# Performance work log

Measured on AMD Instinct MI355X. Metric: run time of the kernel, lower is better.

## Reference

```python
import jax, jax.numpy as jnp
import numpy as np

B, T, E = 4096, 200, 64
VOCAB_ITEM, VOCAB_USER, VOCAB_CTX = 100000, 100000, 10000
DENSE = 16
ATT_H1, ATT_H2 = 64, 32
MLP_H1, MLP_H2 = 256, 128
MLP_IN = E * 4 + DENSE  # 2 sparse feats + item_emb + interest_vec + dense


def _lin(key, fan_in, fan_out):
    k1, k2 = jax.random.split(key)
    s = 1.0 / np.sqrt(fan_in)
    w = jax.random.uniform(k1, (fan_in, fan_out), jnp.float32, -s, s)
    b = jax.random.uniform(k2, (fan_out,), jnp.float32, -s, s)
    return w, b


def setup_inputs() -> dict:
    key = jax.random.key(0)
    ks = jax.random.split(key, 16)
    inp = {}
    inp["target_item"] = jax.random.randint(ks[0], (B,), 0, VOCAB_ITEM)
    inp["history_items"] = jax.random.randint(ks[1], (B, T), 0, VOCAB_ITEM)
    inp["history_mask"] = jax.random.randint(ks[2], (B, T), 0, 2).astype(bool)
    sf_user = jax.random.randint(ks[3], (B, 1), 0, VOCAB_USER)
    sf_ctx = jax.random.randint(ks[4], (B, 1), 0, VOCAB_CTX)
    inp["sparse_features"] = jnp.concatenate([sf_user, sf_ctx], axis=1)
    inp["dense_features"] = jax.random.normal(ks[5], (B, DENSE), jnp.float32)
    # parameters
    inp["item_table"] = jax.random.normal(ks[6], (VOCAB_ITEM, E), jnp.float32)
    inp["user_table"] = jax.random.normal(ks[7], (VOCAB_USER, E), jnp.float32)
    inp["ctx_table"] = jax.random.normal(ks[8], (VOCAB_CTX, E), jnp.float32)
    inp["att_w1"], inp["att_b1"] = _lin(ks[9], 4 * E, ATT_H1)
    inp["att_w2"], inp["att_b2"] = _lin(ks[10], ATT_H1, ATT_H2)
    inp["att_wo"], inp["att_bo"] = _lin(ks[11], ATT_H2, 1)
    inp["mlp_w1"], inp["mlp_b1"] = _lin(ks[12], MLP_IN, MLP_H1)
    inp["mlp_w2"], inp["mlp_b2"] = _lin(ks[13], MLP_H1, MLP_H2)
    inp["out_w"], inp["out_b"] = _lin(ks[14], MLP_H2, 1)
    return inp


def reference(target_item, history_items, history_mask, sparse_features, dense_features,
              item_table, user_table, ctx_table,
              att_w1, att_b1, att_w2, att_b2, att_wo, att_bo,
              mlp_w1, mlp_b1, mlp_w2, mlp_b2, out_w, out_b):
    # embedding lookups
    q = item_table[target_item]               # (B, E)
    keys = item_table[history_items]          # (B, T, E)
    qe = jnp.broadcast_to(q[:, None, :], keys.shape)
    # local activation unit: concat(keys, query, diff, prod) -> small MLP -> score
    attn_in = jnp.concatenate([keys, qe, keys - qe, keys * qe], axis=-1)  # (B, T, 4E)
    h = jax.nn.relu(attn_in @ att_w1 + att_b1)
    h = jax.nn.relu(h @ att_w2 + att_b2)
    scores = (h @ att_wo + att_bo)[..., 0]    # (B, T)
    scores = jnp.where(history_mask, scores, -1e9)
    weights = jax.nn.softmax(scores, axis=-1)
    interest = jnp.einsum('bt,bte->be', weights, keys)  # (B, E)
    # other sparse features
    sp = jnp.concatenate([user_table[sparse_features[:, 0]],
                          ctx_table[sparse_features[:, 1]]], axis=-1)  # (B, 2E)
    mlp_in = jnp.concatenate([sp, q, interest, dense_features], axis=-1)  # (B, 4E+DENSE)
    h = jax.nn.relu(mlp_in @ mlp_w1 + mlp_b1)
    h = jax.nn.relu(h @ mlp_w2 + mlp_b2)
    logits = h @ out_w + out_b                # (B, 1)
    return logits
```

## Files before the change

kernel.cpp:

```cpp
#include <hip/hip_runtime.h>
#include <stdint.h>

#define NB 4096
#define NT 200
#define NE 64

typedef __attribute__((ext_vector_type(8))) __bf16 bf16x8;
typedef __attribute__((ext_vector_type(4))) __bf16 bf16x4;
typedef __attribute__((ext_vector_type(4))) float f32x4;

__device__ __forceinline__ void cvt8(const float4 a, const float4 b,
                                     bf16x8& hi, bf16x8& lo)
{
    float x[8] = {a.x, a.y, a.z, a.w, b.x, b.y, b.z, b.w};
#pragma unroll
    for (int i = 0; i < 8; ++i) {
        const __bf16 h = (__bf16)x[i];
        hi[i] = h;
        lo[i] = (__bf16)(x[i] - (float)h);
    }
}

struct __align__(16) SmemM {
    __bf16 wT_hi[64 * 72];
    __bf16 wT_lo[64 * 72];
    __bf16 w2T_hi[32 * 72];
    __bf16 w2T_lo[32 * 72];
    float  q[64];
    float  biasj[64];
    float  b2[32];
    float  wo[32];
    float  ip[8 * 64];
    float  red_a[8];
    float  red_b[8];
    float  scores[256];
    float  bounce[8][16 * 36];
};

__global__ __launch_bounds__(512)
void din_attn(const int* __restrict__ target_item,
              const int* __restrict__ history_items,
              const int* __restrict__ history_mask,
              const int* __restrict__ sparse_features,
              const float* __restrict__ dense_features,
              const float* __restrict__ item_table,
              const float* __restrict__ user_table,
              const float* __restrict__ ctx_table,
              const float* __restrict__ att_w1,
              const float* __restrict__ att_b1,
              const float* __restrict__ att_w2,
              const float* __restrict__ att_b2,
              const float* __restrict__ att_wo,
              const float* __restrict__ att_bo,
              float* __restrict__ mlp_in)
{
    __shared__ SmemM sm;

    const int b    = blockIdx.x;
    const int tid  = threadIdx.x;
    const int wv   = tid >> 6;
    const int lane = tid & 63;
    const int l15  = lane & 15;
    const int g4   = lane >> 4;

    bf16x8 khi[2][2], klo[2][2];
#pragma unroll
    for (int mt = 0; mt < 2; ++mt) {
        int t = 32 * wv + mt * 16 + l15;
        if (t > NT - 1) t = NT - 1;
        const int hr = history_items[(size_t)b * NT + t];
        const float* kp = item_table + (size_t)hr * NE + g4 * 8;
#pragma unroll
        for (int ks = 0; ks < 2; ++ks) {
            const float4 f0 = *(const float4*)(kp + ks * 32);
            const float4 f1 = *(const float4*)(kp + ks * 32 + 4);
            cvt8(f0, f1, khi[mt][ks], klo[mt][ks]);
        }
    }

    float pre_u = 0.f, pre_c = 0.f, pre_d = 0.f;
    if (tid < NE) {
        pre_u = user_table[(size_t)sparse_features[b * 2 + 0] * NE + tid];
        pre_c = ctx_table[(size_t)sparse_features[b * 2 + 1] * NE + tid];
    } else if (tid < 80) {
        pre_d = dense_features[(size_t)b * 16 + (tid - 64)];
    }

    if (tid < NE) sm.q[tid] = item_table[(size_t)target_item[b] * NE + tid];
    if (tid < 32) { sm.b2[tid] = att_b2[tid]; sm.wo[tid] = att_wo[tid]; }
    const float bo = att_bo[0];
    __syncthreads();

    {
        const int j  = tid & 63;
        const int eb = (tid >> 6) * 8;
        float pb = 0.f;
        bf16x8 vhi, vlo;
#pragma unroll
        for (int i = 0; i < 8; ++i) {
            const int e = eb + i;
            const float qe = sm.q[e];
            const float A  = att_w1[(size_t)(e)       * NE + j];
            const float Bv = att_w1[(size_t)(64 + e)  * NE + j];
            const float C  = att_w1[(size_t)(128 + e) * NE + j];
            const float D  = att_w1[(size_t)(192 + e) * NE + j];
            const float wf = A + C + qe * D;
            const __bf16 h = (__bf16)wf;
            vhi[i] = h;
            vlo[i] = (__bf16)(wf - (float)h);
            pb += qe * (Bv - C);
        }
        *(bf16x8*)(sm.wT_hi + (size_t)j * 72 + eb) = vhi;
        *(bf16x8*)(sm.wT_lo + (size_t)j * 72 + eb) = vlo;
        sm.ip[(tid >> 6) * 64 + j] = pb;
    }
    {
        const int o  = tid & 31;
        const int jb = (tid >> 5) * 4;
        bf16x4 vhi, vlo;
#pragma unroll
        for (int i = 0; i < 4; ++i) {
            const float v = att_w2[(size_t)(jb + i) * 32 + o];
            const __bf16 h = (__bf16)v;
            vhi[i] = h;
            vlo[i] = (__bf16)(v - (float)h);
        }
        *(bf16x4*)(sm.w2T_hi + (size_t)o * 72 + jb) = vhi;
        *(bf16x4*)(sm.w2T_lo + (size_t)o * 72 + jb) = vlo;
    }
    __syncthreads();
    if (tid < NE) {
        float s = att_b1[tid];
#pragma unroll
        for (int w = 0; w < 8; ++w) s += sm.ip[w * 64 + tid];
        sm.biasj[tid] = s;
    }
    __syncthreads();

    f32x4 acc1[2][4];
    {
        const f32x4 z = {0.f, 0.f, 0.f, 0.f};
#pragma unroll
        for (int mt = 0; mt < 2; ++mt)
#pragma unroll
            for (int nt = 0; nt < 4; ++nt) acc1[mt][nt] = z;
    }
#pragma unroll
    for (int nt = 0; nt < 4; ++nt) {
        const __bf16* bph = sm.wT_hi + (nt * 16 + l15) * 72 + g4 * 8;
        const __bf16* bpl = sm.wT_lo + (nt * 16 + l15) * 72 + g4 * 8;
        const bf16x8 bh0 = *(const bf16x8*)(bph);
        const bf16x8 bh1 = *(const bf16x8*)(bph + 32);
        const bf16x8 bl0 = *(const bf16x8*)(bpl);
        const bf16x8 bl1 = *(const bf16x8*)(bpl + 32);
#pragma unroll
        for (int mt = 0; mt < 2; ++mt) {
            f32x4 a = acc1[mt][nt];
            a = __builtin_amdgcn_mfma_f32_16x16x32_bf16(khi[mt][0], bh0, a, 0, 0, 0);
            a = __builtin_amdgcn_mfma_f32_16x16x32_bf16(khi[mt][0], bl0, a, 0, 0, 0);
            a = __builtin_amdgcn_mfma_f32_16x16x32_bf16(klo[mt][0], bh0, a, 0, 0, 0);
            a = __builtin_amdgcn_mfma_f32_16x16x32_bf16(khi[mt][1], bh1, a, 0, 0, 0);
            a = __builtin_amdgcn_mfma_f32_16x16x32_bf16(khi[mt][1], bl1, a, 0, 0, 0);
            a = __builtin_amdgcn_mfma_f32_16x16x32_bf16(klo[mt][1], bh1, a, 0, 0, 0);
            acc1[mt][nt] = a;
        }
    }

#pragma unroll
    for (int nt = 0; nt < 4; ++nt) {
        const float bj = sm.biasj[nt * 16 + l15];
#pragma unroll
        for (int mt = 0; mt < 2; ++mt)
#pragma unroll
            for (int r = 0; r < 4; ++r)
                acc1[mt][nt][r] = fmaxf(acc1[mt][nt][r] + bj, 0.f);
    }

    bf16x8 a2hi[2][2], a2lo[2][2];
    {
        float* bnc = sm.bounce[wv];
#pragma unroll
        for (int mt = 0; mt < 2; ++mt) {
#pragma unroll
            for (int k2s = 0; k2s < 2; ++k2s) {
#pragma unroll
                for (int ntl = 0; ntl < 2; ++ntl) {
                    const int nt = k2s * 2 + ntl;
#pragma unroll
                    for (int r = 0; r < 4; ++r)
                        bnc[(g4 * 4 + r) * 36 + ntl * 16 + l15] = acc1[mt][nt][r];
                }
                const float* rp = bnc + l15 * 36 + g4 * 8;
                const float4 u0 = *(const float4*)(rp);
                const float4 u1 = *(const float4*)(rp + 4);
                cvt8(u0, u1, a2hi[mt][k2s], a2lo[mt][k2s]);
            }
        }
    }

    f32x4 acc2[2][2];
    {
        const f32x4 z = {0.f, 0.f, 0.f, 0.f};
#pragma unroll
        for (int mt = 0; mt < 2; ++mt) { acc2[mt][0] = z; acc2[mt][1] = z; }
    }
#pragma unroll
    for (int nt2 = 0; nt2 < 2; ++nt2) {
        const __bf16* bph = sm.w2T_hi + (nt2 * 16 + l15) * 72 + g4 * 8;
        const __bf16* bpl = sm.w2T_lo + (nt2 * 16 + l15) * 72 + g4 * 8;
        const bf16x8 bh0 = *(const bf16x8*)(bph);
        const bf16x8 bh1 = *(const bf16x8*)(bph + 32);
        const bf16x8 bl0 = *(const bf16x8*)(bpl);
        const bf16x8 bl1 = *(const bf16x8*)(bpl + 32);
#pragma unroll
        for (int mt = 0; mt < 2; ++mt) {
            f32x4 a = acc2[mt][nt2];
            a = __builtin_amdgcn_mfma_f32_16x16x32_bf16(a2hi[mt][0], bh0, a, 0, 0, 0);
            a = __builtin_amdgcn_mfma_f32_16x16x32_bf16(a2hi[mt][0], bl0, a, 0, 0, 0);
            a = __builtin_amdgcn_mfma_f32_16x16x32_bf16(a2lo[mt][0], bh0, a, 0, 0, 0);
            a = __builtin_amdgcn_mfma_f32_16x16x32_bf16(a2hi[mt][1], bh1, a, 0, 0, 0);
            a = __builtin_amdgcn_mfma_f32_16x16x32_bf16(a2hi[mt][1], bl1, a, 0, 0, 0);
            a = __builtin_amdgcn_mfma_f32_16x16x32_bf16(a2lo[mt][1], bh1, a, 0, 0, 0);
            acc2[mt][nt2] = a;
        }
    }

    float sc[2][4];
#pragma unroll
    for (int mt = 0; mt < 2; ++mt)
#pragma unroll
        for (int r = 0; r < 4; ++r) sc[mt][r] = 0.f;
#pragma unroll
    for (int nt2 = 0; nt2 < 2; ++nt2) {
        const float bb = sm.b2[nt2 * 16 + l15];
        const float ww = sm.wo[nt2 * 16 + l15];
#pragma unroll
        for (int mt = 0; mt < 2; ++mt)
#pragma unroll
            for (int r = 0; r < 4; ++r)
                sc[mt][r] += fmaxf(acc2[mt][nt2][r] + bb, 0.f) * ww;
    }
#pragma unroll
    for (int mt = 0; mt < 2; ++mt)
#pragma unroll
        for (int r = 0; r < 4; ++r) {
            float v = sc[mt][r];
            v += __shfl_xor(v, 1);
            v += __shfl_xor(v, 2);
            v += __shfl_xor(v, 4);
            v += __shfl_xor(v, 8);
            sc[mt][r] = v;
        }
    if (l15 == 0) {
#pragma unroll
        for (int mt = 0; mt < 2; ++mt)
#pragma unroll
            for (int r = 0; r < 4; ++r) {
                const int t = 32 * wv + mt * 16 + g4 * 4 + r;
                float val;
                if (t < NT) {
                    const int mk = history_mask[(size_t)b * NT + t];
                    val = (mk != 0) ? (sc[mt][r] + bo) : -1e9f;
                } else {
                    val = -INFINITY;
                }
                sm.scores[t] = val;
            }
    }
    __syncthreads();

    const float v = (tid < 256) ? sm.scores[tid] : -INFINITY;
    float m = v;
#pragma unroll
    for (int s = 32; s; s >>= 1) m = fmaxf(m, __shfl_xor(m, s));
    if (lane == 0) sm.red_a[wv] = m;
    __syncthreads();
    float mx = sm.red_a[0];
#pragma unroll
    for (int w = 1; w < 8; ++w) mx = fmaxf(mx, sm.red_a[w]);
    const float ex = __expf(v - mx);
    float ssum = ex;
#pragma unroll
    for (int s = 32; s; s >>= 1) ssum += __shfl_xor(ssum, s);
    if (lane == 0) sm.red_b[wv] = ssum;
    __syncthreads();
    float total = 0.f;
#pragma unroll
    for (int w = 0; w < 8; ++w) total += sm.red_b[w];
    if (tid < 256) sm.scores[tid] = ex / total;
    __syncthreads();

    {
        const int e = lane;
        float acc = 0.f;
        const int tb = 25 * wv;
#pragma unroll 5
        for (int i = 0; i < 25; ++i) {
            const int t = tb + i;
            const float wt = sm.scores[t];
            const int hr = history_items[(size_t)b * NT + t];
            acc += wt * item_table[(size_t)hr * NE + e];
        }
        sm.ip[wv * 64 + e] = acc;
    }
    __syncthreads();

    float* row = mlp_in + (size_t)b * 272;
    if (tid < NE) {
        float inter = 0.f;
#pragma unroll
        for (int w = 0; w < 8; ++w) inter += sm.ip[w * 64 + tid];
        row[0 + tid]   = pre_u;
        row[64 + tid]  = pre_c;
        row[128 + tid] = sm.q[tid];
        row[192 + tid] = inter;
    } else if (tid >= 64 && tid < 80) {
        row[256 + (tid - 64)] = pre_d;
    }
}

#define MR 2
__global__ __launch_bounds__(256)
void din_mlp(const float* __restrict__ mlp_in,
             const float* __restrict__ w1,
             const float* __restrict__ b1,
             const float* __restrict__ w2,
             const float* __restrict__ b2,
             const float* __restrict__ ow,
             const float* __restrict__ ob,
             float* __restrict__ out)
{
    __shared__ float inT[272 * MR];
    __shared__ float h1T[256 * MR];
    __shared__ float p2[2 * MR * 128];
    __shared__ float h2_lds[MR * 128];

    const int b0  = blockIdx.x * MR;
    const int tid = threadIdx.x;

    for (int i = tid; i < MR * 272; i += 256) {
        const int r = i / 272, k = i - 272 * r;
        inT[k * MR + r] = mlp_in[(size_t)b0 * 272 + i];
    }
    __syncthreads();

    {
        const float bias = b1[tid];
        float a0 = bias, a1 = bias;
        const float2* iT = (const float2*)inT;
#pragma unroll 16
        for (int k = 0; k < 272; ++k) {
            const float wv = w1[(size_t)k * 256 + tid];
            const float2 iv = iT[k];
            a0 += iv.x * wv; a1 += iv.y * wv;
        }
        float2 o;
        o.x = fmaxf(a0, 0.f); o.y = fmaxf(a1, 0.f);
        ((float2*)h1T)[tid] = o;
    }
    __syncthreads();

    {
        const int o = tid & 127, half = tid >> 7;
        float c0 = 0.f, c1 = 0.f;
        const float2* hT = (const float2*)h1T;
#pragma unroll 16
        for (int kk = 0; kk < 128; ++kk) {
            const int k = half * 128 + kk;
            const float wv = w2[(size_t)k * 128 + o];
            const float2 hv = hT[k];
            c0 += hv.x * wv; c1 += hv.y * wv;
        }
        p2[(half * MR + 0) * 128 + o] = c0;
        p2[(half * MR + 1) * 128 + o] = c1;
    }
    __syncthreads();
    if (tid < 128) {
        const float bias = b2[tid];
#pragma unroll
        for (int r = 0; r < MR; ++r)
            h2_lds[r * 128 + tid] =
                fmaxf(p2[r * 128 + tid] + p2[(MR + r) * 128 + tid] + bias, 0.f);
    }
    __syncthreads();

    if (tid < 16 * MR) {
        const int r = tid >> 4, l = tid & 15;
        float a = 0.f;
#pragma unroll
        for (int kk = 0; kk < 8; ++kk) {
            const int k = l * 8 + kk;
            a += h2_lds[r * 128 + k] * ow[k];
        }
        a += __shfl_xor(a, 8, 16);
        a += __shfl_xor(a, 4, 16);
        a += __shfl_xor(a, 2, 16);
        a += __shfl_xor(a, 1, 16);
        if (l == 0) out[b0 + r] = a + ob[0];
    }
}

extern "C" void kernel_launch(void* const* d_in, const int* in_sizes, int n_in,
                              void* d_out, int out_size, void* d_ws, size_t ws_size,
                              hipStream_t stream)
{
    float* mlp_in = (float*)d_ws;

    din_attn<<<NB, 512, 0, stream>>>(
        (const int*)d_in[0],
        (const int*)d_in[1],
        (const int*)d_in[2],
        (const int*)d_in[3],
        (const float*)d_in[4],
        (const float*)d_in[5],
        (const float*)d_in[6],
        (const float*)d_in[7],
        (const float*)d_in[8],  (const float*)d_in[9],
        (const float*)d_in[10], (const float*)d_in[11],
        (const float*)d_in[12], (const float*)d_in[13],
        mlp_in);

    din_mlp<<<NB / MR, 256, 0, stream>>>(
        mlp_in,
        (const float*)d_in[14], (const float*)d_in[15],
        (const float*)d_in[16], (const float*)d_in[17],
        (const float*)d_in[18], (const float*)d_in[19],
        (float*)d_out);
}
```

Baseline: 257.2 us.

## Rewrite DIN output MLP with split-bf16 MFMA over 16-row tiles

The final MLP kernel now processes 16 batch rows per 512-thread block instead of 2 per 256-thread block. Both dense layers run on bf16 MFMA instructions using a hi/lo split of inputs and weights (three MFMAs per step) to keep near-fp32 accuracy. The output dot product is folded into the second layer's epilogue with shuffles. This amortizes each weight read over 16 rows instead of 2 and moves the math onto matrix cores. The cost is converting weights to bf16 on every load and strided per-element weight reads from global memory.

```diff
diff --git a/kernel.cpp b/kernel.cpp
--- a/kernel.cpp
+++ b/kernel.cpp
@@ -13,6 +13,16 @@
                                      bf16x8& hi, bf16x8& lo)
 {
     float x[8] = {a.x, a.y, a.z, a.w, b.x, b.y, b.z, b.w};
+#pragma unroll
+    for (int i = 0; i < 8; ++i) {
+        const __bf16 h = (__bf16)x[i];
+        hi[i] = h;
+        lo[i] = (__bf16)(x[i] - (float)h);
+    }
+}
+
+__device__ __forceinline__ void cvt8a(const float* x, bf16x8& hi, bf16x8& lo)
+{
 #pragma unroll
     for (int i = 0; i < 8; ++i) {
         const __bf16 h = (__bf16)x[i];
@@ -319,8 +329,20 @@
     }
 }
 
-#define MR 2
-__global__ __launch_bounds__(256)
+#define XP 296
+
+struct __align__(16) SmemL {
+    __bf16 xh[16 * XP];
+    __bf16 xl[16 * XP];
+    __bf16 h1h[16 * XP];
+    __bf16 h1l[16 * XP];
+    float  b1v[256];
+    float  b2v[128];
+    float  owv[128];
+    float  part[8][16];
+};
+
+__global__ __launch_bounds__(512)
 void din_mlp(const float* __restrict__ mlp_in,
              const float* __restrict__ w1,
              const float* __restrict__ b1,
@@ -330,73 +352,123 @@
              const float* __restrict__ ob,
              float* __restrict__ out)
 {
-    __shared__ float inT[272 * MR];
-    __shared__ float h1T[256 * MR];
-    __shared__ float p2[2 * MR * 128];
-    __shared__ float h2_lds[MR * 128];
-
-    const int b0  = blockIdx.x * MR;
-    const int tid = threadIdx.x;
-
-    for (int i = tid; i < MR * 272; i += 256) {
-        const int r = i / 272, k = i - 272 * r;
-        inT[k * MR + r] = mlp_in[(size_t)b0 * 272 + i];
-    }
-    __syncthreads();
-
-    {
-        const float bias = b1[tid];
-        float a0 = bias, a1 = bias;
-        const float2* iT = (const float2*)inT;
-#pragma unroll 16
-        for (int k = 0; k < 272; ++k) {
-            const float wv = w1[(size_t)k * 256 + tid];
-            const float2 iv = iT[k];
-            a0 += iv.x * wv; a1 += iv.y * wv;
-        }
-        float2 o;
-        o.x = fmaxf(a0, 0.f); o.y = fmaxf(a1, 0.f);
-        ((float2*)h1T)[tid] = o;
-    }
-    __syncthreads();
-
-    {
-        const int o = tid & 127, half = tid >> 7;
-        float c0 = 0.f, c1 = 0.f;
-        const float2* hT = (const float2*)h1T;
-#pragma unroll 16
-        for (int kk = 0; kk < 128; ++kk) {
-            const int k = half * 128 + kk;
-            const float wv = w2[(size_t)k * 128 + o];
-            const float2 hv = hT[k];
-            c0 += hv.x * wv; c1 += hv.y * wv;
-        }
-        p2[(half * MR + 0) * 128 + o] = c0;
-        p2[(half * MR + 1) * 128 + o] = c1;
-    }
-    __syncthreads();
-    if (tid < 128) {
-        const float bias = b2[tid];
-#pragma unroll
-        for (int r = 0; r < MR; ++r)
-            h2_lds[r * 128 + tid] =
-                fmaxf(p2[r * 128 + tid] + p2[(MR + r) * 128 + tid] + bias, 0.f);
-    }
-    __syncthreads();
-
-    if (tid < 16 * MR) {
-        const int r = tid >> 4, l = tid & 15;
-        float a = 0.f;
-#pragma unroll
-        for (int kk = 0; kk < 8; ++kk) {
-            const int k = l * 8 + kk;
-            a += h2_lds[r * 128 + k] * ow[k];
-        }
-        a += __shfl_xor(a, 8, 16);
-        a += __shfl_xor(a, 4, 16);
-        a += __shfl_xor(a, 2, 16);
-        a += __shfl_xor(a, 1, 16);
-        if (l == 0) out[b0 + r] = a + ob[0];
+    __shared__ SmemL sm;
+
+    const int b0   = blockIdx.x * 16;
+    const int tid  = threadIdx.x;
+    const int wv   = tid >> 6;
+    const int lane = tid & 63;
+    const int l15  = lane & 15;
+    const int g4   = lane >> 4;
+
+    for (int i = tid; i < 16 * XP; i += 512) {
+        const int r = i / XP, k = i - r * XP;
+        const float v = (k < 272) ? mlp_in[(size_t)(b0 + r) * 272 + k] : 0.f;
+        const __bf16 h = (__bf16)v;
+        sm.xh[i] = h;
+        sm.xl[i] = (__bf16)(v - (float)h);
+    }
+    if (tid < 256) sm.b1v[tid] = b1[tid];
+    else if (tid < 384) sm.b2v[tid - 256] = b2[tid - 256];
+    else sm.owv[tid - 384] = ow[tid - 384];
+    __syncthreads();
+
+    f32x4 acc[2];
+    {
+        const f32x4 z = {0.f, 0.f, 0.f, 0.f};
+        acc[0] = z; acc[1] = z;
+    }
+#pragma unroll
+    for (int ks = 0; ks < 9; ++ks) {
+        const bf16x8 ah = *(const bf16x8*)(sm.xh + l15 * XP + ks * 32 + g4 * 8);
+        const bf16x8 al = *(const bf16x8*)(sm.xl + l15 * XP + ks * 32 + g4 * 8);
+#pragma unroll
+        for (int nt = 0; nt < 2; ++nt) {
+            const int n = wv * 32 + nt * 16 + l15;
+            float wf[8];
+            if (ks < 8) {
+#pragma unroll
+                for (int i = 0; i < 8; ++i)
+                    wf[i] = w1[(size_t)(ks * 32 + g4 * 8 + i) * 256 + n];
+            } else {
+#pragma unroll
+                for (int i = 0; i < 8; ++i) wf[i] = 0.f;
+                if (g4 < 2) {
+#pragma unroll
+                    for (int i = 0; i < 8; ++i)
+                        wf[i] = w1[(size_t)(256 + g4 * 8 + i) * 256 + n];
+                }
+            }
+            bf16x8 bh, bl;
+            cvt8a(wf, bh, bl);
+            f32x4 a = acc[nt];
+            a = __builtin_amdgcn_mfma_f32_16x16x32_bf16(ah, bh, a, 0, 0, 0);
+            a = __builtin_amdgcn_mfma_f32_16x16x32_bf16(ah, bl, a, 0, 0, 0);
+            a = __builtin_amdgcn_mfma_f32_16x16x32_bf16(al, bh, a, 0, 0, 0);
+            acc[nt] = a;
+        }
+    }
+
+#pragma unroll
+    for (int nt = 0; nt < 2; ++nt) {
+        const int n = wv * 32 + nt * 16 + l15;
+        const float bias = sm.b1v[n];
+#pragma unroll
+        for (int r = 0; r < 4; ++r) {
+            const float v = fmaxf(acc[nt][r] + bias, 0.f);
+            const __bf16 h = (__bf16)v;
+            sm.h1h[(g4 * 4 + r) * XP + n] = h;
+            sm.h1l[(g4 * 4 + r) * XP + n] = (__bf16)(v - (float)h);
+        }
+    }
+    __syncthreads();
+
+    f32x4 acc2;
+    {
+        const f32x4 z = {0.f, 0.f, 0.f, 0.f};
+        acc2 = z;
+    }
+    const int n2 = wv * 16 + l15;
+#pragma unroll
+    for (int ks = 0; ks < 8; ++ks) {
+        const bf16x8 ah = *(const bf16x8*)(sm.h1h + l15 * XP + ks * 32 + g4 * 8);
+        const bf16x8 al = *(const bf16x8*)(sm.h1l + l15 * XP + ks * 32 + g4 * 8);
+        float wf[8];
+#pragma unroll
+        for (int i = 0; i < 8; ++i)
+            wf[i] = w2[(size_t)(ks * 32 + g4 * 8 + i) * 128 + n2];
+        bf16x8 bh, bl;
+        cvt8a(wf, bh, bl);
+        acc2 = __builtin_amdgcn_mfma_f32_16x16x32_bf16(ah, bh, acc2, 0, 0, 0);
+        acc2 = __builtin_amdgcn_mfma_f32_16x16x32_bf16(ah, bl, acc2, 0, 0, 0);
+        acc2 = __builtin_amdgcn_mfma_f32_16x16x32_bf16(al, bh, acc2, 0, 0, 0);
+    }
+
+    {
+        const float bias = sm.b2v[n2];
+        const float ww   = sm.owv[n2];
+        float s[4];
+#pragma unroll
+        for (int r = 0; r < 4; ++r) {
+            float v = fmaxf(acc2[r] + bias, 0.f) * ww;
+            v += __shfl_xor(v, 1);
+            v += __shfl_xor(v, 2);
+            v += __shfl_xor(v, 4);
+            v += __shfl_xor(v, 8);
+            s[r] = v;
+        }
+        if (l15 == 0) {
+#pragma unroll
+            for (int r = 0; r < 4; ++r)
+                sm.part[wv][g4 * 4 + r] = s[r];
+        }
+    }
+    __syncthreads();
+    if (tid < 16) {
+        float o = ob[0];
+#pragma unroll
+        for (int w = 0; w < 8; ++w) o += sm.part[w][tid];
+        out[b0 + tid] = o;
     }
 }
 
@@ -420,7 +492,7 @@
         (const float*)d_in[12], (const float*)d_in[13],
         mlp_in);
 
-    din_mlp<<<NB / MR, 256, 0, stream>>>(
+    din_mlp<<<NB / 16, 512, 0, stream>>>(
         mlp_in,
         (const float*)d_in[14], (const float*)d_in[15],
         (const float*)d_in[16], (const float*)d_in[17],
```

Measured after the change: 238.5 us. 7.3% less time.
